# Kernel tuning notes

Hardware: AMD Instinct MI355X
Metric: run time of the kernel (lower is better)

Reference implementation:

```python
import jax, jax.numpy as jnp
import numpy as np

J, L, M, N = 4, 8, 256, 256
SLANT = 0.5          # anisotropy of the Morlet envelope (4/L)
EPS = 1e-5           # BatchNorm eps


def _grids(m, n):
    kx = 2.0 * np.pi * np.fft.fftfreq(m)
    ky = 2.0 * np.pi * np.fft.fftfreq(n)
    return kx[:, None], ky[None, :]


def _make_psi(m, n, j):
    # Bank of L zero-mean Morlet band-pass filters at scale j, built in Fourier.
    kx, ky = _grids(m, n)
    sigma = 0.8 * (2.0 ** j)
    xi = (3.0 * np.pi / 4.0) / (2.0 ** j)
    filt = np.empty((L, m, n), np.float32)
    for l in range(L):
        th = l * np.pi / L
        w1 = kx * np.cos(th) + ky * np.sin(th)
        w2 = -kx * np.sin(th) + ky * np.cos(th)
        a = np.exp(-0.5 * sigma ** 2 * ((w1 - xi) ** 2 + (SLANT * w2) ** 2))
        env = np.exp(-0.5 * sigma ** 2 * (w1 ** 2 + (SLANT * w2) ** 2))
        beta = np.exp(-0.5 * sigma ** 2 * xi ** 2)   # enforces psi_hat(0)=0
        f = a - beta * env
        filt[l] = (f / max(f.max(), 1e-12)).astype(np.float32)
    return jnp.asarray(filt)


def _make_phi(m, n, j):
    # Gaussian low-pass at scale j, in Fourier.
    kx, ky = _grids(m, n)
    sigma = 0.8 * (2.0 ** j)
    return jnp.asarray(np.exp(-0.5 * sigma ** 2 * (kx ** 2 + ky ** 2)).astype(np.float32))


# Filters indexed by (resolution r, effective scale js): a scale-j filter applied at
# resolution r equals a scale-(j-r) filter on the 2^r-subsampled grid.
PSI, PHI = {}, {}
for r in range(J):
    m = M >> r
    PHI[r] = _make_phi(m, m, J - r)
    for js in range(0 if r == 0 else 1, J - r):
        PSI[(r, js)] = _make_psi(m, m, js)


def _sub(x, k):
    return x if k == 1 else x[..., ::k, ::k]


def scattering2d(x):
    # x: [B, M, N] real -> [B, 417, 16, 16]
    Xf = jnp.fft.fft2(x)
    s0 = _sub(jnp.fft.ifft2(Xf * PHI[0]).real, 2 ** J)[:, None]
    s1, s2 = [], []
    for j1 in range(J):
        y = jnp.fft.ifft2(Xf[:, None] * PSI[(0, j1)][None])          # [B,L,M,N]
        u1 = _sub(jnp.abs(y), 2 ** j1)                                # [B,L,m1,m1]
        u1f = jnp.fft.fft2(u1)
        s1.append(_sub(jnp.fft.ifft2(u1f * PHI[j1]).real, 2 ** (J - j1)))
        for j2 in range(j1 + 1, J):
            y2 = jnp.fft.ifft2(u1f[:, :, None] * PSI[(j1, j2 - j1)][None, None])  # [B,L,L,m1,m1]
            u2 = _sub(jnp.abs(y2), 2 ** (j2 - j1))                    # [B,L,L,m2,m2]
            s2c = _sub(jnp.fft.ifft2(jnp.fft.fft2(u2) * PHI[j2]).real, 2 ** (J - j2))
            s2.append(s2c.reshape(s2c.shape[0], L * L, M >> J, N >> J))
    return jnp.concatenate([s0] + s1 + s2, axis=1)


def _bn(h, g, b, m, v):
    # BatchNorm1d in eval mode (running stats); Dropout is identity in eval.
    return (h - m) * jax.lax.rsqrt(v + EPS) * g + b


def setup_inputs():
    key = jax.random.key(0)
    ks = jax.random.split(key, 24)
    D = (1 + J * L + L * L * (J * (J - 1) // 2)) * (M >> J) * (N >> J)  # 106752
    B = 16
    inp = {"x": jax.random.normal(ks[0], (B, 1, M, N), jnp.float32)}
    dims = [(D, 1024), (1024, 512), (512, 128), (128, 1)]
    i = 1
    for li, (din, dout) in enumerate(dims, 1):
        inp[f"w{li}"] = jax.random.normal(ks[i], (din, dout), jnp.float32) * 0.02; i += 1
        inp[f"b{li}"] = jax.random.normal(ks[i], (dout,), jnp.float32) * 0.02; i += 1
        if li < 4:
            inp[f"bn{li}g"] = jax.random.uniform(ks[i], (dout,), jnp.float32, minval=0.5, maxval=1.5); i += 1
            inp[f"bn{li}b"] = jax.random.normal(ks[i], (dout,), jnp.float32) * 0.02; i += 1
            inp[f"bn{li}m"] = jnp.zeros((dout,), jnp.float32)
            inp[f"bn{li}v"] = jnp.ones((dout,), jnp.float32)
    return inp


def reference(x, w1, b1, bn1g, bn1b, bn1m, bn1v, w2, b2, bn2g, bn2b, bn2m, bn2v,
              w3, b3, bn3g, bn3b, bn3m, bn3v, w4, b4):
    s = scattering2d(x[:, 0])              # [B,417,16,16]
    h = s.reshape(s.shape[0], -1)          # [B,106752]
    h = _bn(jax.nn.relu(h @ w1 + b1), bn1g, bn1b, bn1m, bn1v)
    h = _bn(jax.nn.relu(h @ w2 + b2), bn2g, bn2b, bn2m, bn2v)
    h = _bn(jax.nn.relu(h @ w3 + b3), bn3g, bn3b, bn3m, bn3v)
    return h @ w4 + b4                     # [B,1]
```

## Files before the change

### kernel.cpp

```cpp
#include <hip/hip_runtime.h>
#include <math.h>
#include <string.h>

#define PI_D 3.14159265358979323846264338327950288


enum { IN_COMPLEX = 0, IN_REAL = 1, IN_MULFOLD = 2 };
enum { OUT_COMPLEX = 0, OUT_ABS = 1, OUT_REAL_S = 2, OUT_COMPLEX_FOLD = 3, OUT_FOLD = 4 };

struct RftParams {
  const float2* srcC;
  const float*  srcR;
  const float*  filt;
  float2* dstC;
  float*  dstR;
  float2* foldDst;
  const float* foldPhi;
  float foldScale;
  int m1;
  int srcDiv;
  int filtMod;
  float scale;
  float sign;
  int chDiv, chBase, b0;
  int inMode, outMode;
};

template<int M>
__global__ __launch_bounds__(256) void rft_kernel(RftParams p) {
  constexpr int R = (M >= 64) ? 8 : ((M == 32) ? 16 : 32);
  constexpr int T = (M == 16) ? 4 : ((M == 32) ? 5 : ((M == 64) ? 6 : ((M == 128) ? 7 : 8)));
  __shared__ float2 Abuf[R][M + 1];
  __shared__ float2 Bbuf[R][M + 1];
  __shared__ float2 W[M / 2];
  __shared__ float red[256][2];
  const int tid = threadIdx.x;
  const long rows0 = (long)blockIdx.x * R;

  {
    const float base = p.sign * 6.28318530717958647692f / (float)M;
    for (int i = tid; i < M / 2; i += 256) {
      float sv, cv;
      sincosf(base * (float)i, &sv, &cv);
      W[i] = make_float2(cv, sv);
    }
  }

  if (p.inMode == IN_COMPLEX) {
    const float2* s = p.srcC + rows0 * M;
    for (int idx = tid; idx < R * M; idx += 256)
      Abuf[idx / M][idx % M] = s[idx];
  } else if (p.inMode == IN_REAL) {
    const float* s = p.srcR + rows0 * M;
    for (int idx = tid; idx < R * M; idx += 256)
      Abuf[idx / M][idx % M] = make_float2(s[idx], 0.f);
  } else {
    const int m1 = p.m1;
    const int k = m1 / M;
    for (int idx = tid; idx < R * M; idx += 256) {
      const int rl = idx / M, c = idx % M;
      const long g = rows0 + rl;
      const long img = g / M;
      const int r = (int)(g - img * M);
      const float2* sp = p.srcC + (img / p.srcDiv) * (long)m1 * m1;
      const float* fp = p.filt + (long)(img % p.filtMod) * m1 * m1;
      float re = 0.f, im = 0.f;
      for (int qr = 0; qr < k; qr++) {
        const long ro = (long)(r + qr * M) * m1;
        const float2* srow = sp + ro;
        const float*  frow = fp + ro;
        for (int qc = 0; qc < k; qc++) {
          const int cc = c + qc * M;
          const float2 v = srow[cc];
          const float fv = frow[cc];
          re = fmaf(v.x, fv, re);
          im = fmaf(v.y, fv, im);
        }
      }
      Abuf[rl][c] = make_float2(re * p.scale, im * p.scale);
    }
  }
  __syncthreads();

  #pragma unroll
  for (int t = 0; t < T; t++) {
    const int s = 1 << t;
    float2 (*Src)[M + 1] = (t & 1) ? Bbuf : Abuf;
    float2 (*Dst)[M + 1] = (t & 1) ? Abuf : Bbuf;
    for (int bf = tid; bf < R * (M / 2); bf += 256) {
      const int row = bf / (M / 2);
      const int j = bf - row * (M / 2);
      const float2 a = Src[row][j];
      const float2 b = Src[row][j + M / 2];
      const float2 w = W[j & ~(s - 1)];
      const float vx = a.x - b.x, vy = a.y - b.y;
      const int dc = (j & (s - 1)) + ((j >> t) << (t + 1));
      Dst[row][dc] = make_float2(a.x + b.x, a.y + b.y);
      Dst[row][dc + s] = make_float2(vx * w.x - vy * w.y, vx * w.y + vy * w.x);
    }
    __syncthreads();
  }
  float2 (*P)[M + 1] = (T & 1) ? Bbuf : Abuf;

  if (p.outMode == OUT_COMPLEX) {
    for (int idx = tid; idx < R * M; idx += 256) {
      const int rl = idx & (R - 1);
      const int fo = idx / R;
      const long g = rows0 + rl;
      const long img = g / M;
      const int rpos = (int)(g - img * M);
      p.dstC[img * (long)M * M + (long)fo * M + rpos] = P[rl][fo];
    }
  } else if (p.outMode == OUT_ABS) {
    for (int idx = tid; idx < R * M; idx += 256) {
      const int rl = idx & (R - 1);
      const int fo = idx / R;
      const long g = rows0 + rl;
      const long img = g / M;
      const int rpos = (int)(g - img * M);
      const float2 z = P[rl][fo];
      p.dstR[img * (long)M * M + (long)fo * M + rpos] = sqrtf(z.x * z.x + z.y * z.y);
    }
  } else if (p.outMode == OUT_REAL_S) {
    for (int idx = tid; idx < R * M; idx += 256) {
      const int rl = idx & (R - 1);
      const int fo = idx / R;
      const long g = rows0 + rl;
      const long img = g / M;
      const int rpos = (int)(g - img * M);
      const int bidx = (int)(img / p.chDiv) + p.b0;
      const int ch = p.chBase + (int)(img % p.chDiv);
      p.dstR[((long)bidx * 417 + ch) * 256 + fo * M + rpos] = P[rl][fo].x;
    }
  } else if (R == 8) {
    const long img0 = rows0 / M;
    const int rbase = (int)(rows0 - img0 * M);
    float ar = 0.f, ai = 0.f;
    for (int idx = tid; idx < R * M; idx += 256) {
      const int rl = idx & 7;
      const int fo = idx >> 3;
      const float2 z = P[rl][fo];
      if (p.outMode == OUT_COMPLEX_FOLD)
        p.dstC[img0 * (long)M * M + (long)fo * M + (rbase + rl)] = z;
      const float ph = p.foldPhi[(long)fo * M + (rbase + rl)] * p.foldScale;
      ar = fmaf(z.x, ph, ar);
      ai = fmaf(z.y, ph, ai);
    }
    red[tid][0] = ar; red[tid][1] = ai;
    __syncthreads();
    if (tid < 128) {
      ar = red[tid][0] + red[tid + 128][0];
      ai = red[tid][1] + red[tid + 128][1];
      const int ro = tid >> 3;
      const int co = (rbase + (tid & 7)) & 15;
      float* fd = (float*)(p.foldDst + img0 * 256 + ro * 16 + co);
      atomicAdd(fd, ar);
      atomicAdd(fd + 1, ai);
    }
  }
}

static void rft_go(int M, int nimg, const RftParams& p, hipStream_t st) {
  const int R = (M >= 64) ? 8 : ((M == 32) ? 16 : 32);
  const int blocks = nimg * M / R;
  switch (M) {
    case 256: rft_kernel<256><<<blocks, 256, 0, st>>>(p); break;
    case 128: rft_kernel<128><<<blocks, 256, 0, st>>>(p); break;
    case  64: rft_kernel< 64><<<blocks, 256, 0, st>>>(p); break;
    case  32: rft_kernel< 32><<<blocks, 256, 0, st>>>(p); break;
    case  16: rft_kernel< 16><<<blocks, 256, 0, st>>>(p); break;
  }
}

template<int N>
__device__ __forceinline__ void stage_rows(float2 (*S_)[N + 1], float2 (*D_)[N + 1],
                                           const float2* W, int t, float sgn) {
  const int tid = threadIdx.x;
  const int s = 1 << t;
  constexpr int half = N / 2;
  for (int bf = tid; bf < N * half; bf += 256) {
    const int row = bf / half;
    const int j = bf - row * half;
    const float2 a = S_[row][j];
    const float2 b = S_[row][j + half];
    const float2 w = W[j & ~(s - 1)];
    const float wy = sgn * w.y;
    const float vx = a.x - b.x, vy = a.y - b.y;
    const int dc = (j & (s - 1)) + ((j >> t) << (t + 1));
    D_[row][dc] = make_float2(a.x + b.x, a.y + b.y);
    D_[row][dc + s] = make_float2(vx * w.x - vy * wy, vx * wy + vy * w.x);
  }
}

template<int N>
__device__ __forceinline__ void stage_cols(float2 (*S_)[N + 1], float2 (*D_)[N + 1],
                                           const float2* W, int t, float sgn) {
  const int tid = threadIdx.x;
  const int s = 1 << t;
  constexpr int half = N / 2;
  for (int bf = tid; bf < N * half; bf += 256) {
    const int col = bf % N;
    const int j = bf / N;
    const float2 a = S_[j][col];
    const float2 b = S_[j + half][col];
    const float2 w = W[j & ~(s - 1)];
    const float wy = sgn * w.y;
    const float vx = a.x - b.x, vy = a.y - b.y;
    const int dr = (j & (s - 1)) + ((j >> t) << (t + 1));
    D_[dr][col] = make_float2(a.x + b.x, a.y + b.y);
    D_[dr + s][col] = make_float2(vx * w.x - vy * wy, vx * wy + vy * w.x);
  }
}

template<int N>
__device__ __forceinline__ void fft2d(float2 (*A)[N + 1], float2 (*B)[N + 1],
                                      const float2* W, float sgn) {
  constexpr int T = (N == 64) ? 6 : ((N == 32) ? 5 : 4);
  for (int t = 0; t < T; t++) {
    if (t & 1) stage_rows<N>(B, A, W, t, sgn); else stage_rows<N>(A, B, W, t, sgn);
    __syncthreads();
  }
  for (int t = 0; t < T; t++) {
    if ((T + t) & 1) stage_cols<N>(B, A, W, t, sgn); else stage_cols<N>(A, B, W, t, sgn);
    __syncthreads();
  }
}

template<int MS, int MI>
__global__ __launch_bounds__(256) void chain_kernel(const float2* __restrict__ src,
                                                    const float* __restrict__ psi,
                                                    const float* __restrict__ phi,
                                                    float2* __restrict__ u1fOut,
                                                    float* __restrict__ S,
                                                    int chBase, int chDiv) {
  __shared__ float2 A[MI][MI + 1];
  __shared__ float2 B[MI][MI + 1];
  __shared__ float2 FA[16][17];
  __shared__ float2 FB[16][17];
  __shared__ float2 W[MI / 2];
  __shared__ float2 W16[8];
  const int tid = threadIdx.x;
  const int img = blockIdx.x;

  for (int i = tid; i < MI / 2; i += 256) {
    float sv, cv;
    sincosf(6.28318530717958647692f * (float)i / (float)MI, &sv, &cv);
    W[i] = make_float2(cv, sv);
  }
  if (tid < 8) W16[tid] = make_float2(cosf(0.39269908169872415481f * (float)tid),
                                      sinf(0.39269908169872415481f * (float)tid));

  constexpr int K = MS / MI;
  const float sc1 = 1.f / (float)(MS * MS);
  const float2* sp = src + (long)(img >> 3) * MS * MS;
  const float* fp = psi + (long)(img & 7) * MS * MS;
  for (int idx = tid; idx < MI * MI; idx += 256) {
    const int r = idx / MI, c = idx - (idx / MI) * MI;
    float re = 0.f, im = 0.f;
    for (int qr = 0; qr < K; qr++) {
      const long ro = (long)(r + qr * MI) * MS;
      for (int qc = 0; qc < K; qc++) {
        const long pos = ro + (c + qc * MI);
        const float2 v = sp[pos];
        const float fv = fp[pos];
        re = fmaf(v.x, fv, re);
        im = fmaf(v.y, fv, im);
      }
    }
    A[r][c] = make_float2(re * sc1, im * sc1);
  }
  __syncthreads();

  fft2d<MI>(A, B, W, 1.f);

  for (int idx = tid; idx < MI * MI; idx += 256) {
    const int r = idx / MI, c = idx - (idx / MI) * MI;
    const float2 z = A[r][c];
    A[r][c] = make_float2(sqrtf(z.x * z.x + z.y * z.y), 0.f);
  }
  __syncthreads();

  fft2d<MI>(A, B, W, -1.f);

  if (u1fOut) {
    for (int idx = tid; idx < MI * MI; idx += 256) {
      const int r = idx / MI, c = idx - (idx / MI) * MI;
      u1fOut[(long)img * MI * MI + idx] = A[r][c];
    }
  }

  {
    constexpr int K2 = MI / 16;
    const float sc2 = 1.f / (float)(MI * MI);
    const int ro = tid >> 4, co = tid & 15;
    float re = 0.f, im = 0.f;
    for (int qr = 0; qr < K2; qr++) {
      const int a_ = ro + qr * 16;
      for (int qc = 0; qc < K2; qc++) {
        const int b_ = co + qc * 16;
        const float2 v = A[a_][b_];
        const float fv = phi[a_ * MI + b_];
        re = fmaf(v.x, fv, re);
        im = fmaf(v.y, fv, im);
      }
    }
    FA[ro][co] = make_float2(re * sc2, im * sc2);
  }
  __syncthreads();

  fft2d<16>(FA, FB, W16, 1.f);

  const long bidx = img / chDiv;
  const int ch = chBase + (img % chDiv);
  S[((long)bidx * 417 + ch) * 256 + tid] = FA[tid >> 4][tid & 15].x;
}

__global__ __launch_bounds__(256) void ifft16_kernel(const float2* __restrict__ spec,
                                                     float* __restrict__ S,
                                                     int chBase, int chDiv) {
  __shared__ float2 FA[16][17];
  __shared__ float2 FB[16][17];
  __shared__ float2 W16[8];
  const int tid = threadIdx.x;
  const int img = blockIdx.x;
  if (tid < 8) W16[tid] = make_float2(cosf(0.39269908169872415481f * (float)tid),
                                      sinf(0.39269908169872415481f * (float)tid));
  FA[tid >> 4][tid & 15] = spec[(long)img * 256 + tid];
  __syncthreads();
  fft2d<16>(FA, FB, W16, 1.f);
  const long bidx = img / chDiv;
  const int ch = chBase + (img % chDiv);
  S[((long)bidx * 417 + ch) * 256 + tid] = FA[tid >> 4][tid & 15].x;
}

__device__ const long PSI_CUM[7] = {524288, 1048576, 1572864, 2097152, 2228224, 2359296, 2392064};
__device__ const int  PSI_MM[7]  = {256, 256, 256, 256, 128, 128, 64};
__device__ const int  PSI_JS[7]  = {0, 1, 2, 3, 1, 2, 1};

__device__ __forceinline__ double dfreq(int i, int m) {
  return (double)((i < (m >> 1)) ? i : i - m) / (double)m;
}

__global__ __launch_bounds__(256) void build_psi_kernel(float* psi, int* fmax) {
  const long i = (long)blockIdx.x * 256 + threadIdx.x;
  int bank = 0;
  while (i >= PSI_CUM[bank]) bank++;
  const long base = bank ? PSI_CUM[bank - 1] : 0;
  const long rem = i - base;
  const int m = PSI_MM[bank], js = PSI_JS[bank];
  const long mm2 = (long)m * m;
  const int l = (int)(rem / mm2);
  const long pos = rem - (long)l * mm2;
  const int r = (int)(pos / m), c = (int)(pos - (long)r * m);
  const double sigma = 0.8 * (double)(1 << js);
  const double xi = (3.0 * PI_D / 4.0) / (double)(1 << js);
  const double th = (double)l * PI_D / 8.0;
  const double kx = 2.0 * PI_D * dfreq(r, m);
  const double ky = 2.0 * PI_D * dfreq(c, m);
  const double ct = cos(th), st = sin(th);
  const double w1 = kx * ct + ky * st;
  const double w2 = -kx * st + ky * ct;
  const double s2 = sigma * sigma;
  const double aa  = exp(-0.5 * s2 * ((w1 - xi) * (w1 - xi) + 0.25 * w2 * w2));
  const double env = exp(-0.5 * s2 * (w1 * w1 + 0.25 * w2 * w2));
  const double beta = exp(-0.5 * s2 * xi * xi);
  const double f = aa - beta * env;
  psi[i] = (float)f;

  float v = fmaxf((float)f, 0.f);
  #pragma unroll
  for (int off = 32; off > 0; off >>= 1)
    v = fmaxf(v, __shfl_down(v, off, 64));
  __shared__ float wmax[4];
  const int lane = threadIdx.x & 63, wid = threadIdx.x >> 6;
  if (lane == 0) wmax[wid] = v;
  __syncthreads();
  if (threadIdx.x == 0) {
    const float mv = fmaxf(fmaxf(wmax[0], wmax[1]), fmaxf(wmax[2], wmax[3]));
    atomicMax(&fmax[bank * 8 + l], __float_as_int(mv));
  }
}

__global__ void norm_psi_kernel(float* psi, const int* fmax) {
  const long i = (long)blockIdx.x * 256 + threadIdx.x;
  if (i >= 2392064L) return;
  int bank = 0;
  while (i >= PSI_CUM[bank]) bank++;
  const long base = bank ? PSI_CUM[bank - 1] : 0;
  const long rem = i - base;
  const int m = PSI_MM[bank];
  const int l = (int)(rem / ((long)m * m));
  const float mx = fmaxf(__int_as_float(fmax[bank * 8 + l]), 1e-12f);
  psi[i] = psi[i] / mx;
}

__global__ void build_phi_kernel(float* phi) {
  const long i = (long)blockIdx.x * 256 + threadIdx.x;
  if (i >= 87040L) return;
  int rr; long base;
  if (i < 65536) { rr = 0; base = 0; }
  else if (i < 81920) { rr = 1; base = 65536; }
  else if (i < 86016) { rr = 2; base = 81920; }
  else { rr = 3; base = 86016; }
  const int m = 256 >> rr;
  const double sigma = 0.8 * (double)(1 << (4 - rr));
  const long pos = i - base;
  const int r = (int)(pos / m), c = (int)(pos % m);
  const double kx = 2.0 * PI_D * dfreq(r, m);
  const double ky = 2.0 * PI_D * dfreq(c, m);
  phi[i] = (float)exp(-0.5 * sigma * sigma * (kx * kx + ky * ky));
}

__global__ __launch_bounds__(256) void mlp1_kernel(const float* __restrict__ S,
                                                   const float* __restrict__ w1,
                                                   float* __restrict__ out1) {
  __shared__ float hs[16][256];
  const int o = blockIdx.x * 256 + threadIdx.x;
  const int ch = blockIdx.y;
  for (int idx = threadIdx.x; idx < 16 * 256; idx += 256) {
    const int b = idx >> 8, kk = idx & 255;
    hs[b][kk] = S[((long)b * 417 + ch) * 256 + kk];
  }
  __syncthreads();
  float acc[16];
  #pragma unroll
  for (int b = 0; b < 16; b++) acc[b] = 0.f;
  const float* wp = w1 + (long)ch * 256 * 1024 + o;
  for (int kk = 0; kk < 256; kk++) {
    const float w = wp[(long)kk * 1024];
    #pragma unroll
    for (int b = 0; b < 16; b++) acc[b] = fmaf(hs[b][kk], w, acc[b]);
  }
  #pragma unroll
  for (int b = 0; b < 16; b++) atomicAdd(&out1[b * 1024 + o], acc[b]);
}

__global__ void l1post_kernel(const float* out1, const float* b1, const float* g,
                              const float* bb, const float* mm, const float* vv, float* h1) {
  const int i = blockIdx.x * 256 + threadIdx.x;
  if (i < 16384) {
    const int o = i & 1023;
    const float xv = fmaxf(out1[i] + b1[o], 0.f);
    const float rs = (float)(1.0 / sqrt((double)vv[o] + 1e-5));
    h1[i] = (xv - mm[o]) * rs * g[o] + bb[o];
  }
}

__global__ __launch_bounds__(256) void mlp2_kernel(const float* h1, const float* w2, const float* b2,
                                                   const float* g, const float* bb, const float* mm,
                                                   const float* vv, float* h2) {
  __shared__ float hs[16][256];
  const int o = blockIdx.x * 256 + threadIdx.x;
  float acc[16];
  #pragma unroll
  for (int b = 0; b < 16; b++) acc[b] = 0.f;
  for (int kc = 0; kc < 4; kc++) {
    __syncthreads();
    for (int idx = threadIdx.x; idx < 16 * 256; idx += 256) {
      const int b = idx >> 8, kk = idx & 255;
      hs[b][kk] = h1[b * 1024 + kc * 256 + kk];
    }
    __syncthreads();
    for (int kk = 0; kk < 256; kk++) {
      const float w = w2[(long)(kc * 256 + kk) * 512 + o];
      #pragma unroll
      for (int b = 0; b < 16; b++) acc[b] = fmaf(hs[b][kk], w, acc[b]);
    }
  }
  const float bias = b2[o], gg = g[o], bbv = bb[o], mv = mm[o];
  const float rs = (float)(1.0 / sqrt((double)vv[o] + 1e-5));
  for (int b = 0; b < 16; b++) {
    const float xv = fmaxf(acc[b] + bias, 0.f);
    h2[b * 512 + o] = (xv - mv) * rs * gg + bbv;
  }
}

__global__ __launch_bounds__(128) void mlp3_kernel(const float* h2, const float* w3, const float* b3,
                                                   const float* g, const float* bb, const float* mm,
                                                   const float* vv, float* h3) {
  __shared__ float hs[16][256];
  const int o = threadIdx.x;
  float acc[16];
  #pragma unroll
  for (int b = 0; b < 16; b++) acc[b] = 0.f;
  for (int kc = 0; kc < 2; kc++) {
    __syncthreads();
    for (int idx = threadIdx.x; idx < 16 * 256; idx += 128) {
      const int b = idx >> 8, kk = idx & 255;
      hs[b][kk] = h2[b * 512 + kc * 256 + kk];
    }
    __syncthreads();
    for (int kk = 0; kk < 256; kk++) {
      const float w = w3[(kc * 256 + kk) * 128 + o];
      #pragma unroll
      for (int b = 0; b < 16; b++) acc[b] = fmaf(hs[b][kk], w, acc[b]);
    }
  }
  const float bias = b3[o], gg = g[o], bbv = bb[o], mv = mm[o];
  const float rs = (float)(1.0 / sqrt((double)vv[o] + 1e-5));
  for (int b = 0; b < 16; b++) {
    const float xv = fmaxf(acc[b] + bias, 0.f);
    h3[b * 128 + o] = (xv - mv) * rs * gg + bbv;
  }
}

__global__ void mlp4_kernel(const float* h3, const float* w4, const float* b4, float* out) {
  const int b = threadIdx.x;
  if (b < 16) {
    double a = 0.0;
    for (int k = 0; k < 128; k++) a += (double)h3[b * 128 + k] * (double)w4[k];
    out[b] = (float)(a + (double)b4[0]);
  }
}

static RftParams rp0() {
  RftParams p;
  memset(&p, 0, sizeof(p));
  p.srcDiv = 1; p.filtMod = 1; p.chDiv = 1;
  p.scale = 1.f; p.sign = -1.f; p.m1 = 0;
  return p;
}

extern "C" void kernel_launch(void* const* d_in, const int* in_sizes, int n_in,
                              void* d_out, int out_size, void* d_ws, size_t ws_size,
                              hipStream_t stream) {
  (void)in_sizes; (void)n_in; (void)out_size; (void)ws_size;
  const float* x    = (const float*)d_in[0];
  const float* w1   = (const float*)d_in[1];
  const float* b1   = (const float*)d_in[2];
  const float* bn1g = (const float*)d_in[3];
  const float* bn1b = (const float*)d_in[4];
  const float* bn1m = (const float*)d_in[5];
  const float* bn1v = (const float*)d_in[6];
  const float* w2   = (const float*)d_in[7];
  const float* b2   = (const float*)d_in[8];
  const float* bn2g = (const float*)d_in[9];
  const float* bn2b = (const float*)d_in[10];
  const float* bn2m = (const float*)d_in[11];
  const float* bn2v = (const float*)d_in[12];
  const float* w3   = (const float*)d_in[13];
  const float* b3   = (const float*)d_in[14];
  const float* bn3g = (const float*)d_in[15];
  const float* bn3b = (const float*)d_in[16];
  const float* bn3m = (const float*)d_in[17];
  const float* bn3v = (const float*)d_in[18];
  const float* w4   = (const float*)d_in[19];
  const float* b4   = (const float*)d_in[20];

  char* ws = (char*)d_ws;
  float2* XF   = (float2*)(ws + 0);
  float2* BUF1 = (float2*)(ws + 8388608);
  float2* BUF2 = (float2*)(ws + 75497472);
  float2* U1F0 = (float2*)(ws + 109051904);
  float2* U1F1 = (float2*)(ws + 176160768);
  float2* U1F2 = (float2*)(ws + 192937984);
  float*  S    = (float*)(ws + 197132288);
  float*  PSI  = (float*)(ws + 203964416);
  float*  PHI  = (float*)(ws + 213532672);
  int*    FMAX = (int*)(ws + 213880832);
  float2* SF   = (float2*)(ws + 213881088);
  float*  OUT1 = (float*)(ws + 216502528);
  float*  H1   = (float*)(ws + 216568064);
  float*  H2   = (float*)(ws + 216633600);
  float*  H3   = (float*)(ws + 216666368);

  float2* SF0  = SF;
  float2* SF1  = SF + 128 * 256;
  float2* SF01 = SF + 256 * 256;

  static const int psioff[7] = {0, 524288, 1048576, 1572864, 2097152, 2228224, 2359296};
  static const int phioff[4] = {0, 65536, 81920, 86016};

  hipMemsetAsync(FMAX, 0, 256, stream);
  hipMemsetAsync(SF, 0, 1280 * 256 * sizeof(float2), stream);
  build_psi_kernel<<<9344, 256, 0, stream>>>(PSI, FMAX);
  norm_psi_kernel<<<9344, 256, 0, stream>>>(PSI, FMAX);
  build_phi_kernel<<<340, 256, 0, stream>>>(PHI);

  { RftParams p = rp0(); p.inMode = IN_REAL; p.srcR = x; p.outMode = OUT_COMPLEX; p.dstC = BUF1; p.sign = -1.f; rft_go(256, 16, p, stream); }
  { RftParams p = rp0(); p.inMode = IN_COMPLEX; p.srcC = BUF1; p.outMode = OUT_COMPLEX; p.dstC = XF; p.sign = -1.f; rft_go(256, 16, p, stream); }

  { RftParams p = rp0(); p.inMode = IN_MULFOLD; p.srcC = XF; p.filt = PHI + phioff[0]; p.m1 = 256; p.srcDiv = 1; p.filtMod = 1; p.scale = 1.f / 65536.f; p.sign = 1.f; p.outMode = OUT_COMPLEX; p.dstC = BUF1; rft_go(16, 16, p, stream); }
  { RftParams p = rp0(); p.inMode = IN_COMPLEX; p.srcC = BUF1; p.sign = 1.f; p.outMode = OUT_REAL_S; p.dstR = S; p.chDiv = 1; p.chBase = 0; p.b0 = 0; rft_go(16, 16, p, stream); }

  for (int j1 = 0; j1 < 2; j1++) {
    const int m1 = 256 >> j1;
    const float isc1 = 1.f / (float)(m1 * m1);
    float2* U  = (j1 == 0) ? U1F0 : U1F1;
    float2* SFj = (j1 == 0) ? SF0 : SF1;
    { RftParams p = rp0(); p.inMode = IN_MULFOLD; p.srcC = XF; p.filt = PSI + psioff[j1]; p.m1 = 256; p.srcDiv = 8; p.filtMod = 8; p.scale = 1.f / 65536.f; p.sign = 1.f; p.outMode = OUT_COMPLEX; p.dstC = BUF1; rft_go(m1, 128, p, stream); }
    { RftParams p = rp0(); p.inMode = IN_COMPLEX; p.srcC = BUF1; p.sign = 1.f; p.outMode = OUT_ABS; p.dstR = (float*)BUF2; rft_go(m1, 128, p, stream); }
    { RftParams p = rp0(); p.inMode = IN_REAL; p.srcR = (const float*)BUF2; p.sign = -1.f; p.outMode = OUT_COMPLEX; p.dstC = BUF1; rft_go(m1, 128, p, stream); }
    { RftParams p = rp0(); p.inMode = IN_COMPLEX; p.srcC = BUF1; p.sign = -1.f; p.outMode = OUT_COMPLEX_FOLD; p.dstC = U;
      p.foldDst = SFj; p.foldPhi = PHI + phioff[j1]; p.foldScale = isc1; rft_go(m1, 128, p, stream); }
    ifft16_kernel<<<128, 256, 0, stream>>>(SFj, S, 1 + 8 * j1, 8);
  }

  chain_kernel<256, 64><<<128, 256, 0, stream>>>(XF, PSI + psioff[2], PHI + phioff[2], U1F2, S, 17, 8);
  chain_kernel<256, 32><<<128, 256, 0, stream>>>(XF, PSI + psioff[3], PHI + phioff[3], nullptr, S, 25, 8);

  for (int cc = 0; cc < 2; cc++) {
    const int b0 = cc * 8;
    const float2* u1fsrc = U1F0 + (long)b0 * 8 * 65536;
    { RftParams p = rp0(); p.inMode = IN_MULFOLD; p.srcC = u1fsrc; p.filt = PSI + psioff[1]; p.m1 = 256; p.srcDiv = 8; p.filtMod = 8; p.scale = 1.f / 65536.f; p.sign = 1.f; p.outMode = OUT_COMPLEX; p.dstC = BUF1; rft_go(128, 512, p, stream); }
    { RftParams p = rp0(); p.inMode = IN_COMPLEX; p.srcC = BUF1; p.sign = 1.f; p.outMode = OUT_ABS; p.dstR = (float*)BUF2; rft_go(128, 512, p, stream); }
    { RftParams p = rp0(); p.inMode = IN_REAL; p.srcR = (const float*)BUF2; p.sign = -1.f; p.outMode = OUT_COMPLEX; p.dstC = BUF1; rft_go(128, 512, p, stream); }
    { RftParams p = rp0(); p.inMode = IN_COMPLEX; p.srcC = BUF1; p.sign = -1.f; p.outMode = OUT_FOLD;
      p.foldDst = SF01 + (long)b0 * 64 * 256; p.foldPhi = PHI + phioff[1]; p.foldScale = 1.f / 16384.f; rft_go(128, 512, p, stream); }
  }
  ifft16_kernel<<<1024, 256, 0, stream>>>(SF01, S, 33, 64);

  chain_kernel<256, 64><<<1024, 256, 0, stream>>>(U1F0, PSI + psioff[2], PHI + phioff[2], nullptr, S,  97, 64);
  chain_kernel<256, 32><<<1024, 256, 0, stream>>>(U1F0, PSI + psioff[3], PHI + phioff[3], nullptr, S, 161, 64);
  chain_kernel<128, 64><<<1024, 256, 0, stream>>>(U1F1, PSI + psioff[4], PHI + phioff[2], nullptr, S, 225, 64);
  chain_kernel<128, 32><<<1024, 256, 0, stream>>>(U1F1, PSI + psioff[5], PHI + phioff[3], nullptr, S, 289, 64);
  chain_kernel< 64, 32><<<1024, 256, 0, stream>>>(U1F2, PSI + psioff[6], PHI + phioff[3], nullptr, S, 353, 64);

  hipMemsetAsync(OUT1, 0, 16 * 1024 * 4, stream);
  mlp1_kernel<<<dim3(4, 417), 256, 0, stream>>>(S, w1, OUT1);
  l1post_kernel<<<64, 256, 0, stream>>>(OUT1, b1, bn1g, bn1b, bn1m, bn1v, H1);
  mlp2_kernel<<<2, 256, 0, stream>>>(H1, w2, b2, bn2g, bn2b, bn2m, bn2v, H2);
  mlp3_kernel<<<1, 128, 0, stream>>>(H2, w3, b3, bn3g, bn3b, bn3m, bn3v, H3);
  mlp4_kernel<<<1, 64, 0, stream>>>(H3, w4, b4, (float*)d_out);
}
```

Baseline: 2.019 ms.

## Share source loads across 8 orientations with fold8 kernel; fuse small MLP and s0 kernels

Result: faster. 1.782 ms (-11.8%).

```diff
diff --git a/kernel.cpp b/kernel.cpp
--- a/kernel.cpp
+++ b/kernel.cpp
@@ -28,8 +28,8 @@
 
 template<int M>
 __global__ __launch_bounds__(256) void rft_kernel(RftParams p) {
-  constexpr int R = (M >= 64) ? 8 : ((M == 32) ? 16 : 32);
-  constexpr int T = (M == 16) ? 4 : ((M == 32) ? 5 : ((M == 64) ? 6 : ((M == 128) ? 7 : 8)));
+  constexpr int R = 8;
+  constexpr int T = (M == 128) ? 7 : 8;
   __shared__ float2 Abuf[R][M + 1];
   __shared__ float2 Bbuf[R][M + 1];
   __shared__ float2 W[M / 2];
@@ -121,18 +121,7 @@
       const float2 z = P[rl][fo];
       p.dstR[img * (long)M * M + (long)fo * M + rpos] = sqrtf(z.x * z.x + z.y * z.y);
     }
-  } else if (p.outMode == OUT_REAL_S) {
-    for (int idx = tid; idx < R * M; idx += 256) {
-      const int rl = idx & (R - 1);
-      const int fo = idx / R;
-      const long g = rows0 + rl;
-      const long img = g / M;
-      const int rpos = (int)(g - img * M);
-      const int bidx = (int)(img / p.chDiv) + p.b0;
-      const int ch = p.chBase + (int)(img % p.chDiv);
-      p.dstR[((long)bidx * 417 + ch) * 256 + fo * M + rpos] = P[rl][fo].x;
-    }
-  } else if (R == 8) {
+  } else {
     const long img0 = rows0 / M;
     const int rbase = (int)(rows0 - img0 * M);
     float ar = 0.f, ai = 0.f;
@@ -161,15 +150,45 @@
 }
 
 static void rft_go(int M, int nimg, const RftParams& p, hipStream_t st) {
-  const int R = (M >= 64) ? 8 : ((M == 32) ? 16 : 32);
-  const int blocks = nimg * M / R;
+  const int blocks = nimg * M / 8;
   switch (M) {
     case 256: rft_kernel<256><<<blocks, 256, 0, st>>>(p); break;
     case 128: rft_kernel<128><<<blocks, 256, 0, st>>>(p); break;
-    case  64: rft_kernel< 64><<<blocks, 256, 0, st>>>(p); break;
-    case  32: rft_kernel< 32><<<blocks, 256, 0, st>>>(p); break;
-    case  16: rft_kernel< 16><<<blocks, 256, 0, st>>>(p); break;
-  }
+  }
+}
+
+template<int M1, int M2>
+__global__ __launch_bounds__(256) void fold8_kernel(const float2* __restrict__ src,
+                                                    const float* __restrict__ filt,
+                                                    float2* __restrict__ out,
+                                                    float scale) {
+  constexpr int K = M1 / M2;
+  constexpr long MM1 = (long)M1 * M1;
+  constexpr int MM2 = M2 * M2;
+  constexpr int PXB = MM2 / 256;
+  const int s = blockIdx.x / PXB;
+  const int px = (blockIdx.x % PXB) * 256 + threadIdx.x;
+  const int r = px / M2, c = px - (px / M2) * M2;
+  const float2* sp = src + (long)s * MM1;
+  float ar[8], ai[8];
+  #pragma unroll
+  for (int l = 0; l < 8; l++) { ar[l] = 0.f; ai[l] = 0.f; }
+  for (int qr = 0; qr < K; qr++) {
+    const int R_ = r + qr * M2;
+    for (int qc = 0; qc < K; qc++) {
+      const long pos = (long)R_ * M1 + (c + qc * M2);
+      const float2 v = sp[pos];
+      #pragma unroll
+      for (int l = 0; l < 8; l++) {
+        const float f = filt[l * MM1 + pos];
+        ar[l] = fmaf(v.x, f, ar[l]);
+        ai[l] = fmaf(v.y, f, ai[l]);
+      }
+    }
+  }
+  #pragma unroll
+  for (int l = 0; l < 8; l++)
+    out[((long)s * 8 + l) * MM2 + px] = make_float2(ar[l] * scale, ai[l] * scale);
 }
 
 template<int N>
@@ -250,24 +269,30 @@
   if (tid < 8) W16[tid] = make_float2(cosf(0.39269908169872415481f * (float)tid),
                                       sinf(0.39269908169872415481f * (float)tid));
 
-  constexpr int K = MS / MI;
-  const float sc1 = 1.f / (float)(MS * MS);
-  const float2* sp = src + (long)(img >> 3) * MS * MS;
-  const float* fp = psi + (long)(img & 7) * MS * MS;
-  for (int idx = tid; idx < MI * MI; idx += 256) {
-    const int r = idx / MI, c = idx - (idx / MI) * MI;
-    float re = 0.f, im = 0.f;
-    for (int qr = 0; qr < K; qr++) {
-      const long ro = (long)(r + qr * MI) * MS;
-      for (int qc = 0; qc < K; qc++) {
-        const long pos = ro + (c + qc * MI);
-        const float2 v = sp[pos];
-        const float fv = fp[pos];
-        re = fmaf(v.x, fv, re);
-        im = fmaf(v.y, fv, im);
+  if (psi == nullptr) {
+    const float2* sp = src + (long)img * MI * MI;
+    for (int idx = tid; idx < MI * MI; idx += 256)
+      A[idx / MI][idx - (idx / MI) * MI] = sp[idx];
+  } else {
+    constexpr int K = MS / MI;
+    const float sc1 = 1.f / (float)(MS * MS);
+    const float2* sp = src + (long)(img >> 3) * MS * MS;
+    const float* fp = psi + (long)(img & 7) * MS * MS;
+    for (int idx = tid; idx < MI * MI; idx += 256) {
+      const int r = idx / MI, c = idx - (idx / MI) * MI;
+      float re = 0.f, im = 0.f;
+      for (int qr = 0; qr < K; qr++) {
+        const long ro = (long)(r + qr * MI) * MS;
+        for (int qc = 0; qc < K; qc++) {
+          const long pos = ro + (c + qc * MI);
+          const float2 v = sp[pos];
+          const float fv = fp[pos];
+          re = fmaf(v.x, fv, re);
+          im = fmaf(v.y, fv, im);
+        }
       }
-    }
-    A[r][c] = make_float2(re * sc1, im * sc1);
+      A[r][c] = make_float2(re * sc1, im * sc1);
+    }
   }
   __syncthreads();
 
@@ -313,6 +338,35 @@
   const long bidx = img / chDiv;
   const int ch = chBase + (img % chDiv);
   S[((long)bidx * 417 + ch) * 256 + tid] = FA[tid >> 4][tid & 15].x;
+}
+
+__global__ __launch_bounds__(256) void s0_kernel(const float2* __restrict__ XF,
+                                                 const float* __restrict__ phi0,
+                                                 float* __restrict__ S) {
+  __shared__ float2 FA[16][17];
+  __shared__ float2 FB[16][17];
+  __shared__ float2 W16[8];
+  const int tid = threadIdx.x;
+  const int img = blockIdx.x;
+  if (tid < 8) W16[tid] = make_float2(cosf(0.39269908169872415481f * (float)tid),
+                                      sinf(0.39269908169872415481f * (float)tid));
+  const int r = tid >> 4, c = tid & 15;
+  const float2* sp = XF + (long)img * 65536;
+  float re = 0.f, im = 0.f;
+  for (int qr = 0; qr < 16; qr++) {
+    const int R_ = r + qr * 16;
+    for (int qc = 0; qc < 16; qc++) {
+      const long pos = (long)R_ * 256 + (c + qc * 16);
+      const float2 v = sp[pos];
+      const float f = phi0[pos];
+      re = fmaf(v.x, f, re);
+      im = fmaf(v.y, f, im);
+    }
+  }
+  FA[r][c] = make_float2(re / 65536.f, im / 65536.f);
+  __syncthreads();
+  fft2d<16>(FA, FB, W16, 1.f);
+  S[((long)img * 417 + 0) * 256 + tid] = FA[r][c].x;
 }
 
 __global__ __launch_bounds__(256) void ifft16_kernel(const float2* __restrict__ spec,
@@ -435,18 +489,11 @@
   for (int b = 0; b < 16; b++) atomicAdd(&out1[b * 1024 + o], acc[b]);
 }
 
-__global__ void l1post_kernel(const float* out1, const float* b1, const float* g,
-                              const float* bb, const float* mm, const float* vv, float* h1) {
-  const int i = blockIdx.x * 256 + threadIdx.x;
-  if (i < 16384) {
-    const int o = i & 1023;
-    const float xv = fmaxf(out1[i] + b1[o], 0.f);
-    const float rs = (float)(1.0 / sqrt((double)vv[o] + 1e-5));
-    h1[i] = (xv - mm[o]) * rs * g[o] + bb[o];
-  }
-}
-
-__global__ __launch_bounds__(256) void mlp2_kernel(const float* h1, const float* w2, const float* b2,
+__global__ __launch_bounds__(256) void mlp2_kernel(const float* __restrict__ out1,
+                                                   const float* __restrict__ b1,
+                                                   const float* __restrict__ g1, const float* __restrict__ bb1,
+                                                   const float* __restrict__ mm1, const float* __restrict__ vv1,
+                                                   const float* w2, const float* b2,
                                                    const float* g, const float* bb, const float* mm,
                                                    const float* vv, float* h2) {
   __shared__ float hs[16][256];
@@ -458,7 +505,10 @@
     __syncthreads();
     for (int idx = threadIdx.x; idx < 16 * 256; idx += 256) {
       const int b = idx >> 8, kk = idx & 255;
-      hs[b][kk] = h1[b * 1024 + kc * 256 + kk];
+      const int feat = kc * 256 + kk;
+      const float xv = fmaxf(out1[b * 1024 + feat] + b1[feat], 0.f);
+      const float rs = (float)(1.0 / sqrt((double)vv1[feat] + 1e-5));
+      hs[b][kk] = (xv - mm1[feat]) * rs * g1[feat] + bb1[feat];
     }
     __syncthreads();
     for (int kk = 0; kk < 256; kk++) {
@@ -475,10 +525,12 @@
   }
 }
 
-__global__ __launch_bounds__(128) void mlp3_kernel(const float* h2, const float* w3, const float* b3,
-                                                   const float* g, const float* bb, const float* mm,
-                                                   const float* vv, float* h3) {
+__global__ __launch_bounds__(128) void mlp34_kernel(const float* h2, const float* w3, const float* b3,
+                                                    const float* g, const float* bb, const float* mm,
+                                                    const float* vv, const float* w4, const float* b4,
+                                                    float* out) {
   __shared__ float hs[16][256];
+  __shared__ float h3s[16][128];
   const int o = threadIdx.x;
   float acc[16];
   #pragma unroll
@@ -500,15 +552,13 @@
   const float rs = (float)(1.0 / sqrt((double)vv[o] + 1e-5));
   for (int b = 0; b < 16; b++) {
     const float xv = fmaxf(acc[b] + bias, 0.f);
-    h3[b * 128 + o] = (xv - mv) * rs * gg + bbv;
-  }
-}
-
-__global__ void mlp4_kernel(const float* h3, const float* w4, const float* b4, float* out) {
-  const int b = threadIdx.x;
-  if (b < 16) {
+    h3s[b][o] = (xv - mv) * rs * gg + bbv;
+  }
+  __syncthreads();
+  if (threadIdx.x < 16) {
+    const int b = threadIdx.x;
     double a = 0.0;
-    for (int k = 0; k < 128; k++) a += (double)h3[b * 128 + k] * (double)w4[k];
+    for (int k = 0; k < 128; k++) a += (double)h3s[b][k] * (double)w4[k];
     out[b] = (float)(a + (double)b4[0]);
   }
 }
@@ -548,21 +598,22 @@
   const float* b4   = (const float*)d_in[20];
 
   char* ws = (char*)d_ws;
-  float2* XF   = (float2*)(ws + 0);
-  float2* BUF1 = (float2*)(ws + 8388608);
-  float2* BUF2 = (float2*)(ws + 75497472);
-  float2* U1F0 = (float2*)(ws + 109051904);
-  float2* U1F1 = (float2*)(ws + 176160768);
-  float2* U1F2 = (float2*)(ws + 192937984);
-  float*  S    = (float*)(ws + 197132288);
-  float*  PSI  = (float*)(ws + 203964416);
-  float*  PHI  = (float*)(ws + 213532672);
-  int*    FMAX = (int*)(ws + 213880832);
-  float2* SF   = (float2*)(ws + 213881088);
-  float*  OUT1 = (float*)(ws + 216502528);
-  float*  H1   = (float*)(ws + 216568064);
-  float*  H2   = (float*)(ws + 216633600);
-  float*  H3   = (float*)(ws + 216666368);
+  const size_t MB = 1048576;
+  float2* XF   = (float2*)(ws + 0 * MB);
+  float2* BUF1 = (float2*)(ws + 8 * MB);
+  float2* BUF2 = (float2*)(ws + 72 * MB);
+  float2* U1F0 = (float2*)(ws + 104 * MB);
+  float2* U1F1 = (float2*)(ws + 168 * MB);
+  float2* U1F2 = (float2*)(ws + 184 * MB);
+  float*  S    = (float*)(ws + 188 * MB);
+  float*  PSI  = (float*)(ws + 195 * MB);
+  float*  PHI  = (float*)(ws + 205 * MB);
+  int*    FMAX = (int*)(ws + 206 * MB);
+  float2* SF   = (float2*)(ws + 207 * MB);
+  float2* G64  = (float2*)(ws + 210 * MB);
+  float2* G32  = (float2*)(ws + 242 * MB);
+  float*  OUT1 = (float*)(ws + 251 * MB);
+  float*  H2   = (float*)(ws + 252 * MB);
 
   float2* SF0  = SF;
   float2* SF1  = SF + 128 * 256;
@@ -580,8 +631,7 @@
   { RftParams p = rp0(); p.inMode = IN_REAL; p.srcR = x; p.outMode = OUT_COMPLEX; p.dstC = BUF1; p.sign = -1.f; rft_go(256, 16, p, stream); }
   { RftParams p = rp0(); p.inMode = IN_COMPLEX; p.srcC = BUF1; p.outMode = OUT_COMPLEX; p.dstC = XF; p.sign = -1.f; rft_go(256, 16, p, stream); }
 
-  { RftParams p = rp0(); p.inMode = IN_MULFOLD; p.srcC = XF; p.filt = PHI + phioff[0]; p.m1 = 256; p.srcDiv = 1; p.filtMod = 1; p.scale = 1.f / 65536.f; p.sign = 1.f; p.outMode = OUT_COMPLEX; p.dstC = BUF1; rft_go(16, 16, p, stream); }
-  { RftParams p = rp0(); p.inMode = IN_COMPLEX; p.srcC = BUF1; p.sign = 1.f; p.outMode = OUT_REAL_S; p.dstR = S; p.chDiv = 1; p.chBase = 0; p.b0 = 0; rft_go(16, 16, p, stream); }
+  s0_kernel<<<16, 256, 0, stream>>>(XF, PHI + phioff[0], S);
 
   for (int j1 = 0; j1 < 2; j1++) {
     const int m1 = 256 >> j1;
@@ -596,8 +646,10 @@
     ifft16_kernel<<<128, 256, 0, stream>>>(SFj, S, 1 + 8 * j1, 8);
   }
 
-  chain_kernel<256, 64><<<128, 256, 0, stream>>>(XF, PSI + psioff[2], PHI + phioff[2], U1F2, S, 17, 8);
-  chain_kernel<256, 32><<<128, 256, 0, stream>>>(XF, PSI + psioff[3], PHI + phioff[3], nullptr, S, 25, 8);
+  fold8_kernel<256, 64><<<16 * 16, 256, 0, stream>>>(XF, PSI + psioff[2], G64, 1.f / 65536.f);
+  chain_kernel<64, 64><<<128, 256, 0, stream>>>(G64, nullptr, PHI + phioff[2], U1F2, S, 17, 8);
+  fold8_kernel<256, 32><<<16 * 4, 256, 0, stream>>>(XF, PSI + psioff[3], G32, 1.f / 65536.f);
+  chain_kernel<32, 32><<<128, 256, 0, stream>>>(G32, nullptr, PHI + phioff[3], nullptr, S, 25, 8);
 
   for (int cc = 0; cc < 2; cc++) {
     const int b0 = cc * 8;
@@ -610,16 +662,20 @@
   }
   ifft16_kernel<<<1024, 256, 0, stream>>>(SF01, S, 33, 64);
 
-  chain_kernel<256, 64><<<1024, 256, 0, stream>>>(U1F0, PSI + psioff[2], PHI + phioff[2], nullptr, S,  97, 64);
-  chain_kernel<256, 32><<<1024, 256, 0, stream>>>(U1F0, PSI + psioff[3], PHI + phioff[3], nullptr, S, 161, 64);
-  chain_kernel<128, 64><<<1024, 256, 0, stream>>>(U1F1, PSI + psioff[4], PHI + phioff[2], nullptr, S, 225, 64);
-  chain_kernel<128, 32><<<1024, 256, 0, stream>>>(U1F1, PSI + psioff[5], PHI + phioff[3], nullptr, S, 289, 64);
-  chain_kernel< 64, 32><<<1024, 256, 0, stream>>>(U1F2, PSI + psioff[6], PHI + phioff[3], nullptr, S, 353, 64);
+  fold8_kernel<256, 64><<<128 * 16, 256, 0, stream>>>(U1F0, PSI + psioff[2], G64, 1.f / 65536.f);
+  chain_kernel<64, 64><<<1024, 256, 0, stream>>>(G64, nullptr, PHI + phioff[2], nullptr, S,  97, 64);
+  fold8_kernel<256, 32><<<128 * 4, 256, 0, stream>>>(U1F0, PSI + psioff[3], G32, 1.f / 65536.f);
+  chain_kernel<32, 32><<<1024, 256, 0, stream>>>(G32, nullptr, PHI + phioff[3], nullptr, S, 161, 64);
+  fold8_kernel<128, 64><<<128 * 16, 256, 0, stream>>>(U1F1, PSI + psioff[4], G64, 1.f / 16384.f);
+  chain_kernel<64, 64><<<1024, 256, 0, stream>>>(G64, nullptr, PHI + phioff[2], nullptr, S, 225, 64);
+  fold8_kernel<128, 32><<<128 * 4, 256, 0, stream>>>(U1F1, PSI + psioff[5], G32, 1.f / 16384.f);
+  chain_kernel<32, 32><<<1024, 256, 0, stream>>>(G32, nullptr, PHI + phioff[3], nullptr, S, 289, 64);
+  fold8_kernel<64, 32><<<128 * 4, 256, 0, stream>>>(U1F2, PSI + psioff[6], G32, 1.f / 4096.f);
+  chain_kernel<32, 32><<<1024, 256, 0, stream>>>(G32, nullptr, PHI + phioff[3], nullptr, S, 353, 64);
 
   hipMemsetAsync(OUT1, 0, 16 * 1024 * 4, stream);
   mlp1_kernel<<<dim3(4, 417), 256, 0, stream>>>(S, w1, OUT1);
-  l1post_kernel<<<64, 256, 0, stream>>>(OUT1, b1, bn1g, bn1b, bn1m, bn1v, H1);
-  mlp2_kernel<<<2, 256, 0, stream>>>(H1, w2, b2, bn2g, bn2b, bn2m, bn2v, H2);
-  mlp3_kernel<<<1, 128, 0, stream>>>(H2, w3, b3, bn3g, bn3b, bn3m, bn3v, H3);
-  mlp4_kernel<<<1, 64, 0, stream>>>(H3, w4, b4, (float*)d_out);
-}
+  mlp2_kernel<<<2, 256, 0, stream>>>(OUT1, b1, bn1g, bn1b, bn1m, bn1v,
+                                     w2, b2, bn2g, bn2b, bn2m, bn2v, H2);
+  mlp34_kernel<<<1, 128, 0, stream>>>(H2, w3, b3, bn3g, bn3b, bn3m, bn3v, w4, b4, (float*)d_out);
+}
```
